# Kernel tuning notes

Hardware: AMD Instinct MI355X
Metric: run time of the kernel (lower is better)

The kernel has to match this reference:

```python
import jax, jax.numpy as jnp
import numpy as np

B, H, W, CIN, C, L = 2, 512, 512, 64, 64, 4
TAU = 1.0


def _conv3x3(x, w):
    # NHWC input, HWIO kernel, SAME zero padding, stride 1 (SignalConv2D corr=True)
    return jax.lax.conv_general_dilated(
        x, w, window_strides=(1, 1), padding='SAME',
        dimension_numbers=('NHWC', 'HWIO', 'NHWC'))


def setup_inputs() -> dict:
    key = jax.random.key(0)
    ks = jax.random.split(key, 10)
    return {
        'x0': jax.random.normal(ks[0], (B, H, W, CIN), jnp.float32),
        'spa_mask': jax.random.uniform(ks[1], (B, H, W, 1), jnp.float32),
        'gumbel_u': jax.random.uniform(ks[2], (1, L, 2, C), jnp.float32),
        'ch_mask': jax.random.uniform(ks[3], (1, L, 2, C), jnp.float32),
        'w0': jax.random.normal(ks[4], (3, 3, CIN, C), jnp.float32) * 0.05,
        'w1': jax.random.normal(ks[5], (3, 3, C, C), jnp.float32) * 0.05,
        'w2': jax.random.normal(ks[6], (3, 3, C, C), jnp.float32) * 0.05,
        'w3': jax.random.normal(ks[7], (3, 3, C, C), jnp.float32) * 0.05,
        'w_collect': jax.random.normal(ks[8], (L * C, C), jnp.float32) * 0.05,
        'b_collect': jnp.zeros((C,), jnp.float32),
    }


def reference(x0, spa_mask, gumbel_u, ch_mask, w0, w1, w2, w3, w_collect, b_collect):
    # Gumbel-softmax channel routing mask over the {dense, sparse} axis (axis=2)
    g = -jnp.log(-jnp.log(jnp.clip(gumbel_u, 1e-10, 1.0)))
    ch = jax.nn.softmax((ch_mask + g) / TAU, axis=2)  # (1, L, 2, C)

    ws = [w0, w1, w2, w3]
    out_feats = []
    fea = x0
    for i in range(L):
        cd = ch[:, i, 0, :][:, None, None, :]  # dense-channel mask  (1,1,1,C)
        cs = ch[:, i, 1, :][:, None, None, :]  # sparse-channel mask (1,1,1,C)
        if i == 0:
            fea = _conv3x3(fea, ws[0])
            fea = fea * cs * spa_mask + fea * cd
        else:
            cdp = ch[:, i - 1, 0, :][:, None, None, :]
            csp = ch[:, i - 1, 1, :][:, None, None, :]
            fea_d = _conv3x3(fea * cdp, ws[i])
            fea_s = _conv3x3(fea * csp, ws[i])
            fea = (fea_d * cs * spa_mask + fea_d * cd
                   + fea_s * cs * spa_mask + fea_s * cd * spa_mask)
        fea = jax.nn.relu(fea)
        out_feats.append(fea)

    cat = jnp.concatenate(out_feats, axis=-1)  # (B, H, W, L*C)
    # 1x1 stride-1 Conv2DTranspose == pointwise linear + bias
    out = jnp.einsum('bhwi,io->bhwo', cat, w_collect) + b_collect
    return out, ch
```

## Files before the change

### kernel.cpp

```cpp
#include <hip/hip_runtime.h>
#include <hip/hip_fp16.h>

#define BB 2
#define HH 512
#define WW 512
#define CC 64
#define PW 514

typedef _Float16 f16;
typedef _Float16 f16x8 __attribute__((ext_vector_type(8)));
typedef float f32x4 __attribute__((ext_vector_type(4)));

static __device__ __forceinline__ f16x8 zero_f16x8() {
    f16x8 z = {(f16)0,(f16)0,(f16)0,(f16)0,(f16)0,(f16)0,(f16)0,(f16)0};
    return z;
}

static __device__ __forceinline__ f16x8 cvt_pair(f32x4 a, f32x4 b) {
    f16x8 o;
    o[0]=(f16)a[0]; o[1]=(f16)a[1]; o[2]=(f16)a[2]; o[3]=(f16)a[3];
    o[4]=(f16)b[0]; o[5]=(f16)b[1]; o[6]=(f16)b[2]; o[7]=(f16)b[3];
    return o;
}

static __device__ __forceinline__ float ch_scale(const float* gum, const float* chm,
                                                 int l, int side, int c) {
    float u0 = gum[(l*2+0)*64+c], u1 = gum[(l*2+1)*64+c];
    u0 = fminf(fmaxf(u0, 1e-10f), 1.0f);
    u1 = fminf(fmaxf(u1, 1e-10f), 1.0f);
    float a0 = chm[(l*2+0)*64+c] - logf(-logf(u0));
    float a1 = chm[(l*2+1)*64+c] - logf(-logf(u1));
    float m = fmaxf(a0, a1);
    float e0 = expf(a0-m), e1 = expf(a1-m);
    float s = e0 + e1;
    return (side == 0) ? e0/s : e1/s;
}

__global__ void k_setup(const float* __restrict__ w0, const float* __restrict__ w1,
                        const float* __restrict__ w2, const float* __restrict__ w3,
                        const float* __restrict__ wc, const float* __restrict__ gum,
                        const float* __restrict__ chm,
                        float* __restrict__ ws_ch, float* __restrict__ out_ch,
                        f16* __restrict__ bpk0, f16* __restrict__ bpkL,
                        f16* __restrict__ wcpk,
                        f16* __restrict__ g1, f16* __restrict__ g2, f16* __restrict__ g3) {
    int idx = blockIdx.x * 256 + threadIdx.x;
    if (idx < 36864) {
        int j = idx & 7, lane = (idx>>3)&63, nb = (idx>>9)&3, kb = idx>>11;
        int k = kb*32 + (lane>>4)*8 + j;
        int tap = k>>6, ci = k&63;
        int co = nb*16 + (lane&15);
        bpk0[idx] = (f16)w0[(tap*64+ci)*64+co];
    } else if (idx < 36864 + 221184) {
        int i2 = idx - 36864;
        int l = i2 / 73728;
        int r = i2 % 73728;
        int j = r&7, lane=(r>>3)&63, nb=(r>>9)&7, kb=r>>12;
        int k = kb*32 + (lane>>4)*8 + j;
        int tap = k>>6, ci = k&63;
        int copr = nb*16 + (lane&15);
        int co = copr & 63;
        const float* w = (l==0)? w1 : (l==1)? w2 : w3;
        float scale = ch_scale(gum, chm, l, (copr < 64) ? 0 : 1, ci);
        bpkL[i2] = (f16)(w[(tap*64+ci)*64+co] * scale);
    } else if (idx < 36864 + 221184 + 16384) {
        int i3 = idx - (36864 + 221184);
        int j=i3&7, lane=(i3>>3)&63, nb=(i3>>9)&3, kb=(i3>>11)&1, l=i3>>12;
        int k = kb*32 + (lane>>4)*8 + j;
        int n = nb*16 + (lane&15);
        wcpk[i3] = (f16)wc[(l*64+k)*64+n];
    } else if (idx < 36864 + 221184 + 16384 + 512) {
        int t = idx - (36864 + 221184 + 16384);
        int l = t >> 7, sc = t & 127;
        int side = sc >> 6, c = sc & 63;
        float v = ch_scale(gum, chm, l, side, c);
        ws_ch[(l*2+side)*64+c] = v;
        out_ch[(l*2+side)*64+c] = v;
    } else {
        int g = idx - (36864 + 221184 + 16384 + 512);
        const int TOT = 2*2052*8;
        if (g >= 3*TOT) return;
        f16* buf = (g < TOT) ? g1 : (g < 2*TOT) ? g2 : g3;
        int e = g % TOT;
        int c8 = e & 7, gg = e >> 3;
        int b = gg / 2052, r = gg % 2052;
        int hp, wp;
        if      (r < 514)  { hp = 0;        wp = r; }
        else if (r < 1028) { hp = 513;      wp = r-514; }
        else if (r < 1540) { hp = r-1027;   wp = 0; }
        else               { hp = r-1539;   wp = 513; }
        *(f16x8*)(buf + ((size_t)(b*PW+hp)*PW + wp)*64 + c8*8) = zero_f16x8();
    }
}

template<int MODE>
__global__ __launch_bounds__(256, 2) void k_conv(const void* __restrict__ in_, f16* __restrict__ out,
        const f16* __restrict__ bpk, const float* __restrict__ ch_l,
        const float* __restrict__ spa) {
    constexpr int NBT = (MODE==0) ? 4 : 8;
    constexpr int NF  = (MODE==0) ? 2 : 4;
    __shared__ f16 smem[4*136*64];
    const int bid = blockIdx.x;
    const int xcd = bid & 7;
    const int wt  = xcd & 3;
    const int b   = xcd >> 2;
    const int hb  = bid >> 3;
    const int h0 = hb*2;
    const int tid = threadIdx.x, lane = tid & 63, wid = tid >> 6;
    const int px0 = wt*128;
    const int sub  = lane & 7;
    const int srel = lane >> 3;
    const int cblk = sub ^ srel;

    if (MODE == 0) {
        const float* inF = (const float*)in_;
        #pragma unroll
        for (int half = 0; half < 2; ++half) {
            const int J0 = half ? 9 : 0;
            const int JN = half ? 8 : 9;
            f32x4 v0[9], v1[9];
            bool ok[9];
            int dst[9];
            #pragma unroll
            for (int t = 0; t < JN; ++t) {
                int j = (J0 + t)*4 + wid;
                int r = j / 17, i = j % 17;
                int s = i*8 + srel;
                int hin = h0 + r - 1;
                int win = px0 + s - 1;
                ok[t] = ((unsigned)hin < HH) && ((unsigned)win < WW);
                dst[t] = r*17408 + i*1024 + lane*16;
                if (ok[t]) {
                    const f32x4* p = (const f32x4*)(inF + (((size_t)(b*HH + hin)*WW + win)*CC + cblk*8));
                    v0[t] = p[0];
                    v1[t] = p[1];
                }
            }
            #pragma unroll
            for (int t = 0; t < JN; ++t) {
                f16x8 o = ok[t] ? cvt_pair(v0[t], v1[t]) : zero_f16x8();
                if ((J0 + t)*4 + wid < 68)
                    *(f16x8*)((char*)smem + dst[t]) = o;
            }
        }
        __syncthreads();
    } else {
        const f16* inH = (const f16*)in_;
        #pragma unroll
        for (int jj = 0; jj < 9; ++jj) {
            int j = jj*4 + wid;
            if (j < 34) {
                int r = j / 17, i = j % 17;
                int s = i*8 + srel;
                const f16* src = inH + ((size_t)(b*PW + h0 + r)*PW + (px0 + s))*64 + cblk*8;
                __builtin_amdgcn_global_load_lds(
                    (const __attribute__((address_space(1))) uint32_t*)src,
                    (__attribute__((address_space(3))) uint32_t*)
                        ((char*)smem + r*17408 + i*1024),
                    16, 0, 0);
            }
        }
        __syncthreads();
        #pragma unroll
        for (int jj = 0; jj < 9; ++jj) {
            int j = 34 + jj*4 + wid;
            if (j < 68) {
                int r = j / 17, i = j % 17;
                int s = i*8 + srel;
                const f16* src = inH + ((size_t)(b*PW + h0 + r)*PW + (px0 + s))*64 + cblk*8;
                __builtin_amdgcn_global_load_lds(
                    (const __attribute__((address_space(1))) uint32_t*)src,
                    (__attribute__((address_space(3))) uint32_t*)
                        ((char*)smem + r*17408 + i*1024),
                    16, 0, 0);
            }
        }
    }

    const int wr = wid >> 1, wn = wid & 1;
    const int lrow = lane & 15, q = lane >> 4;
    const char* smw = (const char*)smem + wr*17408;

    int sb[8][3], po[2][3];
    #pragma unroll
    for (int dxi = 0; dxi < 3; ++dxi) {
        int m7 = (lrow + dxi) & 7;
        po[0][dxi] = ((q)     ^ m7) * 16;
        po[1][dxi] = ((4 + q) ^ m7) * 16;
        #pragma unroll
        for (int mf = 0; mf < 8; ++mf)
            sb[mf][dxi] = (mf*16 + lrow + dxi) * 128;
    }

    f32x4 acc[8][NF];
    #pragma unroll
    for (int i=0;i<8;i++)
        #pragma unroll
        for (int j=0;j<NF;j++) { f32x4 z = {0.f,0.f,0.f,0.f}; acc[i][j] = z; }

    int nbIdx[4];
    nbIdx[0]=wn*2; nbIdx[1]=wn*2+1; nbIdx[2]=wn*2+4; nbIdx[3]=wn*2+5;

    const f16* blane = bpk + (size_t)lane*8;

    f16x8 acur[8], anxt[8], bcur[NF], bnxt[NF];
    #pragma unroll
    for (int nf=0; nf<NF; ++nf)
        bcur[nf] = *reinterpret_cast<const f16x8*>(blane + (size_t)nbIdx[nf]*512);
    #pragma unroll
    for (int mf=0; mf<8; ++mf)
        acur[mf] = *(const f16x8*)(smw + sb[mf][0] + po[0][0]);

    #pragma unroll
    for (int kb = 0; kb < 18; ++kb) {
        if (MODE == 1 && kb == 5) __syncthreads();
        if (kb < 17) {
            const int kn = kb + 1;
            const int rn = kn/6, dxin = (kn%6)/2, halfn = kn & 1;
            #pragma unroll
            for (int nf=0; nf<NF; ++nf)
                bnxt[nf] = *reinterpret_cast<const f16x8*>(blane + (size_t)(kn*NBT + nbIdx[nf])*512);
            #pragma unroll
            for (int mf=0; mf<8; ++mf)
                anxt[mf] = *(const f16x8*)(smw + rn*17408 + sb[mf][dxin] + po[halfn][dxin]);
        }
        __builtin_amdgcn_s_setprio(1);
        #pragma unroll
        for (int nf=0; nf<NF; ++nf) {
            #pragma unroll
            for (int mf=0; mf<8; ++mf)
                acc[mf][nf] = __builtin_amdgcn_mfma_f32_16x16x32_f16(acur[mf], bcur[nf], acc[mf][nf], 0,0,0);
        }
        __builtin_amdgcn_s_setprio(0);
        #pragma unroll
        for (int nf=0; nf<NF; ++nf) bcur[nf] = bnxt[nf];
        #pragma unroll
        for (int mf=0; mf<8; ++mf) acur[mf] = anxt[mf];
    }

    const float* cd = ch_l;
    const float* cs = ch_l + 64;
    const int h = h0 + wr;
    const size_t sparow = (size_t)(b*HH + h)*WW;
    const size_t outrow = (size_t)(b*PW + h + 1)*PW + 1;
    #pragma unroll
    for (int mf=0; mf<8; ++mf) {
        const int pixb = mf*16 + q*4;
        f32x4 sp4 = *(const f32x4*)(spa + sparow + px0 + pixb);
        float sp[4] = {sp4[0], sp4[1], sp4[2], sp4[3]};
        #pragma unroll
        for (int nf2=0; nf2<2; ++nf2) {
            int co = wn*32 + nf2*16 + lrow;
            float vcd = cd[co], vcs = cs[co];
            #pragma unroll
            for (int r=0; r<4; ++r) {
                float v;
                if (MODE==0) v = acc[mf][nf2][r] * (vcs*sp[r] + vcd);
                else         v = acc[mf][nf2][r] * (vcs*sp[r] + vcd) + acc[mf][nf2+2][r] * sp[r];
                v = fmaxf(v, 0.f);
                out[(outrow + px0 + pixb + r)*64 + co] = (f16)v;
            }
        }
    }
}

__global__ __launch_bounds__(256) void k_collect_all(
        const f16* __restrict__ f0, const f16* __restrict__ f1,
        const f16* __restrict__ f2, const f16* __restrict__ f3,
        const f16* __restrict__ wcpk, const float* __restrict__ bias,
        float* __restrict__ out) {
    const int wt = blockIdx.x, h = blockIdx.y, b = blockIdx.z;
    const int tid = threadIdx.x;
    const int lane = tid & 63, wid = tid >> 6;
    const int lrow = lane & 15, lk = (lane>>4)*8;
    const size_t inrow  = (size_t)(b*PW + h + 1)*PW + 1;
    const size_t outrow = (size_t)(b*HH + h)*WW;
    const int px0 = wt*256 + wid*64;

    const f16* feas[4] = {f0, f1, f2, f3};

    f32x4 acc[4][4];
    #pragma unroll
    for (int i=0;i<4;i++)
        #pragma unroll
        for (int j=0;j<4;j++) { f32x4 z = {0.f,0.f,0.f,0.f}; acc[i][j] = z; }

    #pragma unroll
    for (int kb=0; kb<8; ++kb) {
        const f16* fl = feas[kb>>1];
        f16x8 a[4];
        #pragma unroll
        for (int mf=0; mf<4; ++mf)
            a[mf] = *reinterpret_cast<const f16x8*>(fl + (inrow + px0 + mf*16 + lrow)*64 + (kb&1)*32 + lk);
        #pragma unroll
        for (int nf=0; nf<4; ++nf) {
            f16x8 bb = *reinterpret_cast<const f16x8*>(wcpk + ((size_t)(kb*4 + nf)*64 + lane)*8);
            #pragma unroll
            for (int mf=0; mf<4; ++mf)
                acc[mf][nf] = __builtin_amdgcn_mfma_f32_16x16x32_f16(bb, a[mf], acc[mf][nf], 0,0,0);
        }
    }
    const int q = lane >> 4;
    #pragma unroll
    for (int mf=0; mf<4; ++mf) {
        const int pix = px0 + mf*16 + lrow;
        float* orow = out + (outrow + pix)*CC;
        #pragma unroll
        for (int nf=0; nf<4; ++nf) {
            const int co0 = nf*16 + q*4;
            f32x4 b4 = *(const f32x4*)(bias + co0);
            *(f32x4*)(orow + co0) = acc[mf][nf] + b4;
        }
    }
}

template<bool FIRST>
__global__ __launch_bounds__(256) void k_collect(const f16* __restrict__ fea,
        const f16* __restrict__ wcpk_l, const float* __restrict__ bias,
        float* __restrict__ out) {
    const int wt = blockIdx.x, h = blockIdx.y, b = blockIdx.z;
    const int tid = threadIdx.x;
    const int lane = tid & 63, wid = tid >> 6;
    const int lrow = lane & 15, lk = (lane>>4)*8;
    const size_t inrow  = (size_t)(b*PW + h + 1)*PW + 1;
    const size_t outrow = (size_t)(b*HH + h)*WW;
    const int px0 = wt*64 + wid*16;

    f32x4 acc[4];
    #pragma unroll
    for (int j=0;j<4;j++) { f32x4 z = {0.f,0.f,0.f,0.f}; acc[j] = z; }

    #pragma unroll
    for (int kb=0; kb<2; ++kb) {
        f16x8 a = *reinterpret_cast<const f16x8*>(fea + (inrow + px0 + lrow)*64 + kb*32 + lk);
        #pragma unroll
        for (int nf=0; nf<4; ++nf) {
            f16x8 bb = *reinterpret_cast<const f16x8*>(wcpk_l + ((size_t)(kb*4 + nf)*64 + lane)*8);
            acc[nf] = __builtin_amdgcn_mfma_f32_16x16x32_f16(bb, a, acc[nf], 0,0,0);
        }
    }
    const int q = lane >> 4;
    const int pix = px0 + lrow;
    float* orow = out + (outrow + pix)*CC;
    #pragma unroll
    for (int nf=0; nf<4; ++nf) {
        const int co0 = nf*16 + q*4;
        f32x4 v = acc[nf];
        #pragma unroll
        for (int r=0;r<4;++r) {
            float x = v[r];
            if (FIRST) x += bias[co0+r];
            else       x += orow[co0+r];
            orow[co0+r] = x;
        }
    }
}

extern "C" void kernel_launch(void* const* d_in, const int* in_sizes, int n_in,
                              void* d_out, int out_size, void* d_ws, size_t ws_size,
                              hipStream_t stream) {
    const float* x0  = (const float*)d_in[0];
    const float* spa = (const float*)d_in[1];
    const float* gum = (const float*)d_in[2];
    const float* chm = (const float*)d_in[3];
    const float* w0  = (const float*)d_in[4];
    const float* w1  = (const float*)d_in[5];
    const float* w2  = (const float*)d_in[6];
    const float* w3  = (const float*)d_in[7];
    const float* wc  = (const float*)d_in[8];
    const float* bias= (const float*)d_in[9];
    float* out = (float*)d_out;

    char* ws = (char*)d_ws;
    const size_t WBASE = (1u<<20);
    const size_t FB = 67699712ull;
    const size_t NEED_A = WBASE + 4*FB;
    const size_t NEED_B = WBASE + 2*FB;
    if (ws_size < NEED_B) return;

    float* ws_ch = (float*)ws;
    f16* bpk0 = (f16*)(ws + 4096);
    f16* bpkL = (f16*)(ws + 4096 + 73728);
    f16* wcpk = (f16*)(ws + 4096 + 73728 + 442368);

    dim3 gcv(2048, 1, 1);
    dim3 gca(2, 512, 2);
    dim3 gcf(8, 512, 2);
    const int SETUP_GRID = (36864 + 221184 + 16384 + 512 + 3*32832 + 255) / 256;

    if (ws_size >= NEED_A) {
        f16* R0 = (f16*)(ws + WBASE);
        f16* R1 = (f16*)(ws + WBASE + FB);
        f16* R2 = (f16*)(ws + WBASE + 2*FB);
        f16* R3 = (f16*)(ws + WBASE + 3*FB);
        k_setup<<<SETUP_GRID, 256, 0, stream>>>(w0, w1, w2, w3, wc, gum, chm,
                ws_ch, out + 33554432, bpk0, bpkL, wcpk, R1, R2, R3);
        k_conv<0><<<gcv, 256, 0, stream>>>(x0, R1, bpk0,          ws_ch + 0,   spa);
        k_conv<1><<<gcv, 256, 0, stream>>>(R1, R2, bpkL + 0,      ws_ch + 128, spa);
        k_conv<1><<<gcv, 256, 0, stream>>>(R2, R3, bpkL + 73728,  ws_ch + 256, spa);
        k_conv<1><<<gcv, 256, 0, stream>>>(R3, R0, bpkL + 147456, ws_ch + 384, spa);
        k_collect_all<<<gca, 256, 0, stream>>>(R1, R2, R3, R0, wcpk, bias, out);
    } else {
        f16* P0 = (f16*)(ws + WBASE);
        f16* P1 = (f16*)(ws + WBASE + FB);
        k_setup<<<SETUP_GRID, 256, 0, stream>>>(w0, w1, w2, w3, wc, gum, chm,
                ws_ch, out + 33554432, bpk0, bpkL, wcpk, P0, P1, P0);
        k_conv<0><<<gcv, 256, 0, stream>>>(x0, P1, bpk0,          ws_ch + 0,   spa);
        k_collect<true ><<<gcf, 256, 0, stream>>>(P1, wcpk + 0,     bias, out);
        k_conv<1><<<gcv, 256, 0, stream>>>(P1, P0, bpkL + 0,      ws_ch + 128, spa);
        k_collect<false><<<gcf, 256, 0, stream>>>(P0, wcpk + 4096,  bias, out);
        k_conv<1><<<gcv, 256, 0, stream>>>(P0, P1, bpkL + 73728,  ws_ch + 256, spa);
        k_collect<false><<<gcf, 256, 0, stream>>>(P1, wcpk + 8192,  bias, out);
        k_conv<1><<<gcv, 256, 0, stream>>>(P1, P0, bpkL + 147456, ws_ch + 384, spa);
        k_collect<false><<<gcf, 256, 0, stream>>>(P0, wcpk + 12288, bias, out);
    }
}
```

Before: 341.9 us.

## Fuse final conv layer with 1x1 collect projection via shared-memory staging

Adds a MODE 2 conv variant that computes the last 3x3 layer with transposed MFMA operands, so its output lands in shared memory in swizzled layout. The 1x1 collect GEMM then runs in the same kernel, reading earlier layers' features from global memory and the last layer from LDS. This removes one full fp16 feature-map write and re-read and a separate kernel launch, and reduces workspace needs by one buffer. The cost is extra register and LDS pressure in the fused kernel plus additional synchronisation.

```diff
diff --git a/kernel.cpp b/kernel.cpp
--- a/kernel.cpp
+++ b/kernel.cpp
@@ -9,6 +9,7 @@
 
 typedef _Float16 f16;
 typedef _Float16 f16x8 __attribute__((ext_vector_type(8)));
+typedef _Float16 f16x4 __attribute__((ext_vector_type(4)));
 typedef float f32x4 __attribute__((ext_vector_type(4)));
 
 static __device__ __forceinline__ f16x8 zero_f16x8() {
@@ -96,7 +97,10 @@
 template<int MODE>
 __global__ __launch_bounds__(256, 2) void k_conv(const void* __restrict__ in_, f16* __restrict__ out,
         const f16* __restrict__ bpk, const float* __restrict__ ch_l,
-        const float* __restrict__ spa) {
+        const float* __restrict__ spa,
+        const f16* __restrict__ fA, const f16* __restrict__ fB,
+        const f16* __restrict__ wcpk, const float* __restrict__ bias,
+        float* __restrict__ outF) {
     constexpr int NBT = (MODE==0) ? 4 : 8;
     constexpr int NF  = (MODE==0) ? 2 : 4;
     __shared__ f16 smem[4*136*64];
@@ -213,7 +217,7 @@
 
     #pragma unroll
     for (int kb = 0; kb < 18; ++kb) {
-        if (MODE == 1 && kb == 5) __syncthreads();
+        if (MODE >= 1 && kb == 5) __syncthreads();
         if (kb < 17) {
             const int kn = kb + 1;
             const int rn = kn/6, dxin = (kn%6)/2, halfn = kn & 1;
@@ -228,8 +232,12 @@
         #pragma unroll
         for (int nf=0; nf<NF; ++nf) {
             #pragma unroll
-            for (int mf=0; mf<8; ++mf)
-                acc[mf][nf] = __builtin_amdgcn_mfma_f32_16x16x32_f16(acur[mf], bcur[nf], acc[mf][nf], 0,0,0);
+            for (int mf=0; mf<8; ++mf) {
+                if (MODE == 2)
+                    acc[mf][nf] = __builtin_amdgcn_mfma_f32_16x16x32_f16(bcur[nf], acur[mf], acc[mf][nf], 0,0,0);
+                else
+                    acc[mf][nf] = __builtin_amdgcn_mfma_f32_16x16x32_f16(acur[mf], bcur[nf], acc[mf][nf], 0,0,0);
+            }
         }
         __builtin_amdgcn_s_setprio(0);
         #pragma unroll
@@ -242,74 +250,105 @@
     const float* cs = ch_l + 64;
     const int h = h0 + wr;
     const size_t sparow = (size_t)(b*HH + h)*WW;
-    const size_t outrow = (size_t)(b*PW + h + 1)*PW + 1;
-    #pragma unroll
-    for (int mf=0; mf<8; ++mf) {
-        const int pixb = mf*16 + q*4;
-        f32x4 sp4 = *(const f32x4*)(spa + sparow + px0 + pixb);
-        float sp[4] = {sp4[0], sp4[1], sp4[2], sp4[3]};
-        #pragma unroll
-        for (int nf2=0; nf2<2; ++nf2) {
-            int co = wn*32 + nf2*16 + lrow;
-            float vcd = cd[co], vcs = cs[co];
-            #pragma unroll
-            for (int r=0; r<4; ++r) {
-                float v;
-                if (MODE==0) v = acc[mf][nf2][r] * (vcs*sp[r] + vcd);
-                else         v = acc[mf][nf2][r] * (vcs*sp[r] + vcd) + acc[mf][nf2+2][r] * sp[r];
-                v = fmaxf(v, 0.f);
-                out[(outrow + px0 + pixb + r)*64 + co] = (f16)v;
-            }
-        }
-    }
-}
-
-__global__ __launch_bounds__(256) void k_collect_all(
-        const f16* __restrict__ f0, const f16* __restrict__ f1,
-        const f16* __restrict__ f2, const f16* __restrict__ f3,
-        const f16* __restrict__ wcpk, const float* __restrict__ bias,
-        float* __restrict__ out) {
-    const int wt = blockIdx.x, h = blockIdx.y, b = blockIdx.z;
-    const int tid = threadIdx.x;
-    const int lane = tid & 63, wid = tid >> 6;
-    const int lrow = lane & 15, lk = (lane>>4)*8;
-    const size_t inrow  = (size_t)(b*PW + h + 1)*PW + 1;
-    const size_t outrow = (size_t)(b*HH + h)*WW;
-    const int px0 = wt*256 + wid*64;
-
-    const f16* feas[4] = {f0, f1, f2, f3};
-
-    f32x4 acc[4][4];
-    #pragma unroll
-    for (int i=0;i<4;i++)
-        #pragma unroll
-        for (int j=0;j<4;j++) { f32x4 z = {0.f,0.f,0.f,0.f}; acc[i][j] = z; }
-
-    #pragma unroll
-    for (int kb=0; kb<8; ++kb) {
-        const f16* fl = feas[kb>>1];
-        f16x8 a[4];
-        #pragma unroll
-        for (int mf=0; mf<4; ++mf)
-            a[mf] = *reinterpret_cast<const f16x8*>(fl + (inrow + px0 + mf*16 + lrow)*64 + (kb&1)*32 + lk);
-        #pragma unroll
-        for (int nf=0; nf<4; ++nf) {
-            f16x8 bb = *reinterpret_cast<const f16x8*>(wcpk + ((size_t)(kb*4 + nf)*64 + lane)*8);
-            #pragma unroll
-            for (int mf=0; mf<4; ++mf)
-                acc[mf][nf] = __builtin_amdgcn_mfma_f32_16x16x32_f16(bb, a[mf], acc[mf][nf], 0,0,0);
-        }
-    }
-    const int q = lane >> 4;
-    #pragma unroll
-    for (int mf=0; mf<4; ++mf) {
-        const int pix = px0 + mf*16 + lrow;
-        float* orow = out + (outrow + pix)*CC;
-        #pragma unroll
-        for (int nf=0; nf<4; ++nf) {
-            const int co0 = nf*16 + q*4;
-            f32x4 b4 = *(const f32x4*)(bias + co0);
-            *(f32x4*)(orow + co0) = acc[mf][nf] + b4;
+
+    if (MODE != 2) {
+        const size_t outrow = (size_t)(b*PW + h + 1)*PW + 1;
+        #pragma unroll
+        for (int mf=0; mf<8; ++mf) {
+            const int pixb = mf*16 + q*4;
+            f32x4 sp4 = *(const f32x4*)(spa + sparow + px0 + pixb);
+            float sp[4] = {sp4[0], sp4[1], sp4[2], sp4[3]};
+            #pragma unroll
+            for (int nf2=0; nf2<2; ++nf2) {
+                int co = wn*32 + nf2*16 + lrow;
+                float vcd = cd[co], vcs = cs[co];
+                #pragma unroll
+                for (int r=0; r<4; ++r) {
+                    float v;
+                    if (MODE==0) v = acc[mf][nf2][r] * (vcs*sp[r] + vcd);
+                    else         v = acc[mf][nf2][r] * (vcs*sp[r] + vcd) + acc[mf][nf2+2][r] * sp[r];
+                    v = fmaxf(v, 0.f);
+                    out[(outrow + px0 + pixb + r)*64 + co] = (f16)v;
+                }
+            }
+        }
+        return;
+    }
+
+    __syncthreads();
+    {
+        #pragma unroll
+        for (int mf=0; mf<8; ++mf) {
+            const int pix = mf*16 + lrow;
+            const float sp = spa[sparow + px0 + pix];
+            #pragma unroll
+            for (int nf2=0; nf2<2; ++nf2) {
+                const int co0 = wn*32 + nf2*16 + q*4;
+                f32x4 cd4 = *(const f32x4*)(cd + co0);
+                f32x4 cs4 = *(const f32x4*)(cs + co0);
+                f16x4 o;
+                #pragma unroll
+                for (int r=0; r<4; ++r) {
+                    float v = acc[mf][nf2][r] * (cs4[r]*sp + cd4[r]) + acc[mf][nf2+2][r] * sp;
+                    o[r] = (f16)fmaxf(v, 0.f);
+                }
+                const int chunk = co0 >> 3;
+                const int addr = (wr*128 + pix)*128 + ((chunk ^ (pix & 7))*16) + (q & 1)*8;
+                *(f16x4*)((char*)smem + addr) = o;
+            }
+        }
+    }
+    __syncthreads();
+
+    {
+        const int row2 = wid >> 1;
+        const int pxc  = (wid & 1)*64;
+        const int h2 = h0 + row2;
+        const size_t inrow2  = (size_t)(b*PW + h2 + 1)*PW + 1;
+        const size_t outrow2 = (size_t)(b*HH + h2)*WW;
+        const int lk = q*8;
+        const f16* inH = (const f16*)in_;
+
+        f32x4 acc2[4][4];
+        #pragma unroll
+        for (int i=0;i<4;i++)
+            #pragma unroll
+            for (int j=0;j<4;j++) { f32x4 z = {0.f,0.f,0.f,0.f}; acc2[i][j] = z; }
+
+        #pragma unroll
+        for (int kb=0; kb<8; ++kb) {
+            f16x8 a[4];
+            if (kb < 6) {
+                const f16* fl = (kb < 2) ? fA : (kb < 4) ? fB : inH;
+                #pragma unroll
+                for (int mf2=0; mf2<4; ++mf2)
+                    a[mf2] = *reinterpret_cast<const f16x8*>(fl + (inrow2 + px0 + pxc + mf2*16 + lrow)*64 + (kb&1)*32 + lk);
+            } else {
+                const int chunk = (kb-6)*4 + q;
+                #pragma unroll
+                for (int mf2=0; mf2<4; ++mf2) {
+                    const int pixl = pxc + mf2*16 + lrow;
+                    a[mf2] = *(const f16x8*)((const char*)smem + (row2*128 + pixl)*128 + ((chunk ^ (lrow & 7))*16));
+                }
+            }
+            #pragma unroll
+            for (int nf=0; nf<4; ++nf) {
+                f16x8 bb = *reinterpret_cast<const f16x8*>(wcpk + ((size_t)(kb*4 + nf)*64 + lane)*8);
+                #pragma unroll
+                for (int mf2=0; mf2<4; ++mf2)
+                    acc2[mf2][nf] = __builtin_amdgcn_mfma_f32_16x16x32_f16(bb, a[mf2], acc2[mf2][nf], 0,0,0);
+            }
+        }
+        #pragma unroll
+        for (int mf2=0; mf2<4; ++mf2) {
+            const int pixg = px0 + pxc + mf2*16 + lrow;
+            float* orow = outF + (outrow2 + pixg)*CC;
+            #pragma unroll
+            for (int nf=0; nf<4; ++nf) {
+                const int co0 = nf*16 + q*4;
+                f32x4 b4 = *(const f32x4*)(bias + co0);
+                *(f32x4*)(orow + co0) = acc2[mf2][nf] + b4;
+            }
         }
     }
 }
@@ -374,7 +413,7 @@
     char* ws = (char*)d_ws;
     const size_t WBASE = (1u<<20);
     const size_t FB = 67699712ull;
-    const size_t NEED_A = WBASE + 4*FB;
+    const size_t NEED_A = WBASE + 3*FB;
     const size_t NEED_B = WBASE + 2*FB;
     if (ws_size < NEED_B) return;
 
@@ -384,34 +423,39 @@
     f16* wcpk = (f16*)(ws + 4096 + 73728 + 442368);
 
     dim3 gcv(2048, 1, 1);
-    dim3 gca(2, 512, 2);
     dim3 gcf(8, 512, 2);
     const int SETUP_GRID = (36864 + 221184 + 16384 + 512 + 3*32832 + 255) / 256;
 
     if (ws_size >= NEED_A) {
-        f16* R0 = (f16*)(ws + WBASE);
-        f16* R1 = (f16*)(ws + WBASE + FB);
-        f16* R2 = (f16*)(ws + WBASE + 2*FB);
-        f16* R3 = (f16*)(ws + WBASE + 3*FB);
+        f16* R1 = (f16*)(ws + WBASE);
+        f16* R2 = (f16*)(ws + WBASE + FB);
+        f16* R3 = (f16*)(ws + WBASE + 2*FB);
         k_setup<<<SETUP_GRID, 256, 0, stream>>>(w0, w1, w2, w3, wc, gum, chm,
                 ws_ch, out + 33554432, bpk0, bpkL, wcpk, R1, R2, R3);
-        k_conv<0><<<gcv, 256, 0, stream>>>(x0, R1, bpk0,          ws_ch + 0,   spa);
-        k_conv<1><<<gcv, 256, 0, stream>>>(R1, R2, bpkL + 0,      ws_ch + 128, spa);
-        k_conv<1><<<gcv, 256, 0, stream>>>(R2, R3, bpkL + 73728,  ws_ch + 256, spa);
-        k_conv<1><<<gcv, 256, 0, stream>>>(R3, R0, bpkL + 147456, ws_ch + 384, spa);
-        k_collect_all<<<gca, 256, 0, stream>>>(R1, R2, R3, R0, wcpk, bias, out);
+        k_conv<0><<<gcv, 256, 0, stream>>>(x0, R1, bpk0,          ws_ch + 0,   spa,
+                nullptr, nullptr, nullptr, nullptr, nullptr);
+        k_conv<1><<<gcv, 256, 0, stream>>>(R1, R2, bpkL + 0,      ws_ch + 128, spa,
+                nullptr, nullptr, nullptr, nullptr, nullptr);
+        k_conv<1><<<gcv, 256, 0, stream>>>(R2, R3, bpkL + 73728,  ws_ch + 256, spa,
+                nullptr, nullptr, nullptr, nullptr, nullptr);
+        k_conv<2><<<gcv, 256, 0, stream>>>(R3, nullptr, bpkL + 147456, ws_ch + 384, spa,
+                R1, R2, wcpk, bias, out);
     } else {
         f16* P0 = (f16*)(ws + WBASE);
         f16* P1 = (f16*)(ws + WBASE + FB);
         k_setup<<<SETUP_GRID, 256, 0, stream>>>(w0, w1, w2, w3, wc, gum, chm,
                 ws_ch, out + 33554432, bpk0, bpkL, wcpk, P0, P1, P0);
-        k_conv<0><<<gcv, 256, 0, stream>>>(x0, P1, bpk0,          ws_ch + 0,   spa);
+        k_conv<0><<<gcv, 256, 0, stream>>>(x0, P1, bpk0,          ws_ch + 0,   spa,
+                nullptr, nullptr, nullptr, nullptr, nullptr);
         k_collect<true ><<<gcf, 256, 0, stream>>>(P1, wcpk + 0,     bias, out);
-        k_conv<1><<<gcv, 256, 0, stream>>>(P1, P0, bpkL + 0,      ws_ch + 128, spa);
+        k_conv<1><<<gcv, 256, 0, stream>>>(P1, P0, bpkL + 0,      ws_ch + 128, spa,
+                nullptr, nullptr, nullptr, nullptr, nullptr);
         k_collect<false><<<gcf, 256, 0, stream>>>(P0, wcpk + 4096,  bias, out);
-        k_conv<1><<<gcv, 256, 0, stream>>>(P0, P1, bpkL + 73728,  ws_ch + 256, spa);
+        k_conv<1><<<gcv, 256, 0, stream>>>(P0, P1, bpkL + 73728,  ws_ch + 256, spa,
+                nullptr, nullptr, nullptr, nullptr, nullptr);
         k_collect<false><<<gcf, 256, 0, stream>>>(P1, wcpk + 8192,  bias, out);
-        k_conv<1><<<gcv, 256, 0, stream>>>(P1, P0, bpkL + 147456, ws_ch + 384, spa);
+        k_conv<1><<<gcv, 256, 0, stream>>>(P1, P0, bpkL + 147456, ws_ch + 384, spa,
+                nullptr, nullptr, nullptr, nullptr, nullptr);
         k_collect<false><<<gcf, 256, 0, stream>>>(P0, wcpk + 12288, bias, out);
     }
 }
```

Result: faster. 320.4 us (-6.3%).
